# Performance work log

Measured on AMD Instinct MI355X. Metric: run time of the kernel, lower is better.

## Reference

```python
import jax, jax.numpy as jnp
import numpy as np

L = 3          # levels
B = 128        # batch
T0 = 256       # bottom-level sequence length
FACTOR = 4     # tmp_abs_factor -> T levels = [256, 64, 16]
STOCH = 128
DETER = 1024
EMBED = 512
OBS_D = 512    # obs_embed_size / enc_dense_embed_size


def setup_inputs() -> dict:
    key = jax.random.key(0)
    ks = jax.random.split(key, 16)
    w = lambda k, shape: jax.random.normal(k, shape, jnp.float32) * 0.02
    return {
        'obs_l0': jax.random.normal(ks[0], (B, T0, OBS_D), jnp.float32),
        'obs_l1': jax.random.normal(ks[1], (B, T0 // FACTOR, OBS_D), jnp.float32),
        'obs_l2': jax.random.normal(ks[2], (B, T0 // FACTOR**2, OBS_D), jnp.float32),
        # prior input dense: concat(prev_sample, context) -> embed
        'Wp': w(ks[3], (L, STOCH + DETER, EMBED)),
        'bp': jnp.zeros((L, EMBED), jnp.float32),
        # GRUCell (torch semantics): input=embed, hidden=deter
        'Wih': w(ks[4], (L, EMBED, 3 * DETER)),
        'Whh': w(ks[5], (L, DETER, 3 * DETER)),
        'bih': jnp.zeros((L, 3 * DETER), jnp.float32),
        'bhh': jnp.zeros((L, 3 * DETER), jnp.float32),
        # posterior dense: concat(det_out, obs) -> embed, then mean head -> stoch
        'Wq': w(ks[6], (L, DETER + OBS_D, EMBED)),
        'bq': jnp.zeros((L, EMBED), jnp.float32),
        'Wqm': w(ks[7], (L, EMBED, STOCH)),
        'bqm': jnp.zeros((L, STOCH), jnp.float32),
    }


def _gru(x, h, Wih, Whh, bih, bhh):
    # torch.nn.GRUCell math
    gi = x @ Wih + bih
    gh = h @ Whh + bhh
    ir, iz, inn = jnp.split(gi, 3, axis=-1)
    hr, hz, hn = jnp.split(gh, 3, axis=-1)
    r = jax.nn.sigmoid(ir + hr)
    z = jax.nn.sigmoid(iz + hz)
    n = jnp.tanh(inn + r * hn)
    return (1.0 - z) * n + z * h


def _run_level(obs, ctx, p):
    # one RSSMCell scanned over time; returns posterior det_out [B, T, DETER]
    Wp, bp, Wih, Whh, bih, bhh, Wq, bq, Wqm, bqm = p
    bsz = obs.shape[0]

    def step(carry, xt):
        sample, det = carry                       # [B,STOCH], [B,DETER]
        obs_t, ctx_t = xt                         # [B,OBS_D], [B,DETER]
        # prior: dense -> GRU (mean_only, so prior heads don't affect the state path)
        h = jax.nn.relu(jnp.concatenate([sample, ctx_t], -1) @ Wp + bp)
        det_new = _gru(h, det, Wih, Whh, bih, bhh)
        # posterior (use_observation=True): mean head gives next sample (mean_only cell)
        qh = jax.nn.relu(jnp.concatenate([det_new, obs_t], -1) @ Wq + bq)
        qm = qh @ Wqm + bqm
        return (qm, det_new), det_new

    init = (jnp.zeros((bsz, STOCH), obs.dtype), jnp.zeros((bsz, DETER), obs.dtype))
    xs = (jnp.swapaxes(obs, 0, 1), jnp.swapaxes(ctx, 0, 1))  # time-major
    _, dets = jax.lax.scan(step, init, xs)
    return jnp.swapaxes(dets, 0, 1)


def reference(obs_l0, obs_l1, obs_l2, Wp, bp, Wih, Whh, bih, bhh, Wq, bq, Wqm, bqm):
    obs = [obs_l0, obs_l1, obs_l2]
    bsz = obs_l0.shape[0]
    # top-level context is zeros of det-state size
    ctx = jnp.zeros((bsz, obs[L - 1].shape[1], DETER), obs_l0.dtype)
    for level in range(L - 1, -1, -1):
        o = obs[level]
        T = o.shape[1]
        if ctx.shape[1] < T:
            reps = -(-T // ctx.shape[1])  # ceil, matches torch repeat-then-slice
            ctx = jnp.tile(ctx, (1, reps, 1))[:, :T]
        ctx = ctx[:, :T]
        p = (Wp[level], bp[level], Wih[level], Whh[level], bih[level], bhh[level],
             Wq[level], bq[level], Wqm[level], bqm[level])
        ctx = _run_level(o, ctx, p)  # posterior det_out becomes next context
    return ctx  # output_bot_level [B, T0, DETER]
```

## Files before the change

kernel.cpp:

```cpp
#include <hip/hip_runtime.h>
#include <math.h>
#include <cstddef>

#define G3 3072

__device__ __forceinline__ float sigmoidf_(float x){ return 1.0f/(1.0f+expf(-x)); }

__global__ __launch_bounds__(256)
void zero_k(float* p, int n){
    int i = blockIdx.x*blockDim.x + threadIdx.x;
    for (int j = i; j < n; j += gridDim.x*blockDim.x) p[j] = 0.f;
}

__global__ __launch_bounds__(256)
void gemm_k(const float* __restrict__ A, long lda,
            const float* __restrict__ Bm, long ldb,
            const float* __restrict__ bias,
            float* __restrict__ C, long ldc, int K)
{
    __shared__ float xs[16][64];
    const int tid = threadIdx.x;
    const int nl = tid & 31, bl = tid >> 5;
    const int n  = blockIdx.x*64 + nl*2;
    const int m0 = blockIdx.y*16;
    float a0x=0.f,a0y=0.f,a1x=0.f,a1y=0.f;
    for (int kc = 0; kc < K; kc += 64) {
        __syncthreads();
        { int r = tid >> 4, c = (tid & 15)*4;
          *(float4*)&xs[r][c] = *(const float4*)&A[(size_t)(m0+r)*lda + kc + c]; }
        __syncthreads();
        #pragma unroll 8
        for (int kk = 0; kk < 64; ++kk) {
            const float2 w = *(const float2*)&Bm[(size_t)(kc+kk)*ldb + n];
            const float xa = xs[bl][kk], xb = xs[bl+8][kk];
            a0x += xa*w.x; a0y += xa*w.y;
            a1x += xb*w.x; a1y += xb*w.y;
        }
    }
    float bx=0.f, by=0.f;
    if (bias){ bx = bias[n]; by = bias[n+1]; }
    float* c0 = &C[(size_t)(m0+bl)*ldc + n];
    float* c1 = &C[(size_t)(m0+bl+8)*ldc + n];
    c0[0]=a0x+bx; c0[1]=a0y+by; c1[0]=a1x+bx; c1[1]=a1y+by;
}

__global__ __launch_bounds__(512)
void bps_k(const float* __restrict__ bqm, const float* __restrict__ Wps,
           const float* __restrict__ bp, float* __restrict__ bps)
{
    const int n = threadIdx.x;
    float a = 0.f;
    #pragma unroll 8
    for (int k = 0; k < 128; ++k) a += bqm[k]*Wps[(size_t)k*512 + n];
    bps[n] = a + bp[n];
}

__global__ __launch_bounds__(256)
void qh_part_k(const float* __restrict__ det, long ld_det,
               const float* __restrict__ obs, long ld_obs,
               const float* __restrict__ Wq,
               float* __restrict__ qp)
{
    __shared__ float xs[8][256];
    const int tid = threadIdx.x;
    const int nl = tid & 31, mg = tid >> 5;
    const int n  = blockIdx.x*64 + nl*2;
    const int m0 = blockIdx.y*8;
    const int cz = blockIdx.z;
    const float* As; long lda; int kr0;
    if (cz < 4) { As = det + cz*256;     lda = ld_det; kr0 = cz*256; }
    else        { As = obs + (cz-4)*256; lda = ld_obs; kr0 = 1024 + (cz-4)*256; }
    {
        const int r = tid >> 5, c = (tid & 31)*8;
        const float* src = &As[(size_t)(m0+r)*lda + c];
        *(float4*)&xs[r][c]   = *(const float4*)&src[0];
        *(float4*)&xs[r][c+4] = *(const float4*)&src[4];
    }
    __syncthreads();
    const float* w = &Wq[(size_t)kr0*512 + n];
    float ax=0.f, ay=0.f;
    #pragma unroll 8
    for (int kk = 0; kk < 256; ++kk) {
        const float2 wv = *(const float2*)&w[(size_t)kk*512];
        const float x = xs[mg][kk];
        ax += x*wv.x; ay += x*wv.y;
    }
    *(float2*)&qp[(size_t)cz*65536 + (size_t)(m0+mg)*512 + n] = make_float2(ax, ay);
}

__global__ __launch_bounds__(256)
void h_part_k(const float* __restrict__ qp, const float* __restrict__ bq,
              const float* __restrict__ Wqs, float* __restrict__ hp)
{
    __shared__ float xs[8][128];
    const int tid = threadIdx.x;
    const int nl = tid & 31, mg = tid >> 5;
    const int n  = blockIdx.x*64 + nl*2;
    const int m0 = blockIdx.y*8;
    const int kz = blockIdx.z;
    {
        const int r = tid >> 5, c = (tid & 31)*4;
        const int kg = kz*128 + c;
        float4 s = *(const float4*)&bq[kg];
        #pragma unroll
        for (int cc = 0; cc < 6; ++cc) {
            const float4 p = *(const float4*)&qp[(size_t)cc*65536 + (size_t)(m0+r)*512 + kg];
            s.x += p.x; s.y += p.y; s.z += p.z; s.w += p.w;
        }
        s.x = fmaxf(s.x,0.f); s.y = fmaxf(s.y,0.f);
        s.z = fmaxf(s.z,0.f); s.w = fmaxf(s.w,0.f);
        *(float4*)&xs[r][c] = s;
    }
    __syncthreads();
    const float* w = &Wqs[(size_t)(kz*128)*512 + n];
    float ax=0.f, ay=0.f;
    #pragma unroll 8
    for (int kk = 0; kk < 128; ++kk) {
        const float2 wv = *(const float2*)&w[(size_t)kk*512];
        const float x = xs[mg][kk];
        ax += x*wv.x; ay += x*wv.y;
    }
    *(float2*)&hp[(size_t)kz*65536 + (size_t)(m0+mg)*512 + n] = make_float2(ax, ay);
}

__global__ __launch_bounds__(256)
void gru_part_k(const float* __restrict__ hp,
                const float* __restrict__ hc, long ld_hc,
                const float* __restrict__ hbias,
                const float* __restrict__ det, long ld_det,
                const float* __restrict__ Wih, const float* __restrict__ Whh,
                float* __restrict__ giP, float* __restrict__ ghP)
{
    __shared__ float xs[32*132];
    const int tid = threadIdx.x;
    const int nl = tid & 31, mg = tid >> 5;
    const int n  = blockIdx.x*128 + nl*4;
    const int m0 = blockIdx.y*32;
    const int zc = blockIdx.z;
    const bool is_gi = (zc < 4);
    {
        const int r = tid >> 3, c0 = (tid & 7)*16;
        if (is_gi) {
            const int kb = zc*128;
            #pragma unroll
            for (int i = 0; i < 4; ++i) {
                const int c = c0 + i*4, kg = kb + c;
                float4 s = *(const float4*)&hbias[kg];
                if (hc) {
                    const float4 p = *(const float4*)&hc[(size_t)(m0+r)*ld_hc + kg];
                    s.x+=p.x; s.y+=p.y; s.z+=p.z; s.w+=p.w;
                }
                if (hp) {
                    #pragma unroll
                    for (int cc = 0; cc < 4; ++cc) {
                        const float4 p = *(const float4*)&hp[(size_t)cc*65536 + (size_t)(m0+r)*512 + kg];
                        s.x+=p.x; s.y+=p.y; s.z+=p.z; s.w+=p.w;
                    }
                }
                s.x=fmaxf(s.x,0.f); s.y=fmaxf(s.y,0.f);
                s.z=fmaxf(s.z,0.f); s.w=fmaxf(s.w,0.f);
                *(float4*)&xs[r*132 + c] = s;
            }
        } else {
            const int kb = (zc-4)*128;
            #pragma unroll
            for (int i = 0; i < 4; ++i) {
                const int c = c0 + i*4;
                *(float4*)&xs[r*132 + c] =
                    *(const float4*)&det[(size_t)(m0+r)*ld_det + kb + c];
            }
        }
    }
    __syncthreads();
    const float* W; float* outp;
    if (is_gi) { W = Wih + (size_t)(zc*128)*G3 + n;     outp = giP + (size_t)zc*393216; }
    else       { W = Whh + (size_t)((zc-4)*128)*G3 + n; outp = ghP + (size_t)(zc-4)*393216; }
    float4 acc[4];
    #pragma unroll
    for (int j = 0; j < 4; ++j) acc[j] = make_float4(0.f,0.f,0.f,0.f);
    const int rb = mg*4;
    #pragma unroll 2
    for (int kc4 = 0; kc4 < 128; kc4 += 4) {
        float4 xv[4];
        #pragma unroll
        for (int j = 0; j < 4; ++j)
            xv[j] = *(const float4*)&xs[(rb+j)*132 + kc4];
        #pragma unroll
        for (int kk = 0; kk < 4; ++kk) {
            const float4 wv = *(const float4*)&W[(size_t)(kc4+kk)*G3];
            #pragma unroll
            for (int j = 0; j < 4; ++j) {
                const float xj = (kk==0) ? xv[j].x : (kk==1) ? xv[j].y
                               : (kk==2) ? xv[j].z : xv[j].w;
                acc[j].x += xj*wv.x; acc[j].y += xj*wv.y;
                acc[j].z += xj*wv.z; acc[j].w += xj*wv.w;
            }
        }
    }
    #pragma unroll
    for (int j = 0; j < 4; ++j)
        *(float4*)&outp[(size_t)(m0+rb+j)*G3 + n] = acc[j];
}

__global__ __launch_bounds__(256)
void gru_epi_k(const float* __restrict__ giP, const float* __restrict__ ghP,
               const float* __restrict__ bih, const float* __restrict__ bhh,
               const float* __restrict__ det_in, long ld_det,
               float* __restrict__ det_out, long ld_out)
{
    const int d = blockIdx.x*256 + threadIdx.x;
    const int b = blockIdx.y;
    float gir=0.f, giz=0.f, gin=0.f;
    #pragma unroll
    for (int c = 0; c < 4; ++c) {
        const float* p = &giP[(size_t)c*393216 + (size_t)b*G3 + d];
        gir += p[0]; giz += p[1024]; gin += p[2048];
    }
    float ghr=0.f, ghz=0.f, ghn=0.f;
    #pragma unroll
    for (int c = 0; c < 8; ++c) {
        const float* p = &ghP[(size_t)c*393216 + (size_t)b*G3 + d];
        ghr += p[0]; ghz += p[1024]; ghn += p[2048];
    }
    const float r  = sigmoidf_(gir + ghr + bih[d] + bhh[d]);
    const float z  = sigmoidf_(giz + ghz + bih[1024+d] + bhh[1024+d]);
    const float nn = tanhf(gin + bih[2048+d] + r*(ghn + bhh[2048+d]));
    const float dold = det_in[(size_t)b*ld_det + d];
    det_out[(size_t)b*ld_out + d] = (1.f - z)*nn + z*dold;
}

extern "C" void kernel_launch(void* const* d_in, const int* in_sizes, int n_in,
                              void* d_out, int out_size, void* d_ws, size_t ws_size,
                              hipStream_t stream)
{
    const float* obs0 = (const float*)d_in[0];
    const float* obs1 = (const float*)d_in[1];
    const float* obs2 = (const float*)d_in[2];
    const float* Wp   = (const float*)d_in[3];
    const float* bp   = (const float*)d_in[4];
    const float* Wih  = (const float*)d_in[5];
    const float* Whh  = (const float*)d_in[6];
    const float* bih  = (const float*)d_in[7];
    const float* bhh  = (const float*)d_in[8];
    const float* Wq   = (const float*)d_in[9];
    const float* bq   = (const float*)d_in[10];
    const float* Wqm  = (const float*)d_in[11];
    const float* bqm  = (const float*)d_in[12];

    float* ws = (float*)d_ws;
    float* det0 = ws;  ws += (size_t)128*1024;
    float* WqsA = ws;  ws += (size_t)3*512*512;
    float* bpsA = ws;  ws += (size_t)3*512;
    float* dets2= ws;  ws += (size_t)128*16*1024;
    float* dets1= ws;  ws += (size_t)128*64*1024;
    float* HCu  = ws;  ws += (size_t)128*64*512;
    float* qp   = ws;  ws += (size_t)6*128*512;
    float* hp   = ws;  ws += (size_t)4*128*512;
    float* giP  = ws;  ws += (size_t)4*128*3072;
    float* ghP  = ws;  ws += (size_t)8*128*3072;

    zero_k<<<dim3(128), dim3(256), 0, stream>>>(det0, 128*1024);

    for (int l = 0; l < 3; ++l) {
        const float* Wp_l = Wp + (size_t)l*1152*512;
        gemm_k<<<dim3(8,32), dim3(256), 0, stream>>>(
            Wqm + (size_t)l*512*128, 128, Wp_l, 512, nullptr,
            WqsA + (size_t)l*512*512, 512, 128);
        bps_k<<<dim3(1), dim3(512), 0, stream>>>(
            bqm + (size_t)l*128, Wp_l, bp + (size_t)l*512, bpsA + (size_t)l*512);
    }

    const float* obsv[3] = {obs0, obs1, obs2};
    const int Tv[3] = {256, 64, 16};

    for (int level = 2; level >= 0; --level) {
        const int T = Tv[level];
        const float* o = obsv[level];
        float* dseq = (level == 0) ? (float*)d_out : (level == 1 ? dets1 : dets2);
        const float* ctxd = (level == 2) ? nullptr : (level == 1 ? dets2 : dets1);
        const int Tc = (level == 1) ? 16 : 64;

        const float* Wp_l  = Wp  + (size_t)level*1152*512;
        const float* Wpc_l = Wp_l + (size_t)128*512;
        const float* bp_l  = bp  + (size_t)level*512;
        const float* Wih_l = Wih + (size_t)level*512*3072;
        const float* Whh_l = Whh + (size_t)level*1024*3072;
        const float* bih_l = bih + (size_t)level*3072;
        const float* bhh_l = bhh + (size_t)level*3072;
        const float* Wq_l  = Wq  + (size_t)level*1536*512;
        const float* bq_l  = bq  + (size_t)level*512;
        const float* Wqs_l = WqsA + (size_t)level*512*512;
        const float* bps_l = bpsA + (size_t)level*512;

        if (level < 2) {
            gemm_k<<<dim3(8, (128*Tc)/16), dim3(256), 0, stream>>>(
                ctxd, 1024, Wpc_l, 512, nullptr, HCu, 512, 1024);
        }

        for (int t = 0; t < T; ++t) {
            if (t > 0) {
                qh_part_k<<<dim3(8,16,6), dim3(256), 0, stream>>>(
                    dseq + (size_t)(t-1)*1024, (long)T*1024,
                    o + (size_t)(t-1)*512,  (long)T*512, Wq_l, qp);
                h_part_k<<<dim3(8,16,4), dim3(256), 0, stream>>>(qp, bq_l, Wqs_l, hp);
            }
            const float* hc_t  = (level < 2) ? HCu + (size_t)(t % Tc)*512 : nullptr;
            const float* dprev = t ? dseq + (size_t)(t-1)*1024 : det0;
            const long   ldprev = t ? (long)T*1024 : 1024L;
            gru_part_k<<<dim3(24,4,12), dim3(256), 0, stream>>>(
                t ? hp : nullptr, hc_t, (long)Tc*512,
                t ? bps_l : bp_l, dprev, ldprev,
                Wih_l, Whh_l, giP, ghP);
            gru_epi_k<<<dim3(4,128), dim3(256), 0, stream>>>(
                giP, ghP, bih_l, bhh_l, dprev, ldprev,
                dseq + (size_t)t*1024, (long)T*1024);
        }
    }
}
```

Measured before the change: 23.47 ms.

## Move Whh GEMM into stepA and fuse GRU epilogue via last-block atomic counter

The recurrent h@Whh partial GEMM now runs in the same launch as the posterior qh GEMM, since both depend only on the previous det state. That shortens the dependent chain before the Wih GEMM. The GRU epilogue is folded into the Wih GEMM kernel: the last block to finish each output tile, detected with an atomic counter, reduces the partials and applies the gates. This removes one launch per step and the det0 zero buffer. The qh and h kernels are widened to float4 per thread. The cost is a single block doing a serial epilogue per tile, plus atomic and fence overhead.

```diff
diff --git a/kernel.cpp b/kernel.cpp
--- a/kernel.cpp
+++ b/kernel.cpp
@@ -5,6 +5,17 @@
 #define G3 3072
 
 __device__ __forceinline__ float sigmoidf_(float x){ return 1.0f/(1.0f+expf(-x)); }
+
+__device__ __forceinline__ float gru_out_(float gi_r,float gh_r,float bir,float bhr,
+                                          float gi_z,float gh_z,float biz,float bhz,
+                                          float gi_n,float gh_n,float bin,float bhn,
+                                          float dold)
+{
+    const float r = sigmoidf_(gi_r + gh_r + bir + bhr);
+    const float z = sigmoidf_(gi_z + gh_z + biz + bhz);
+    const float n = tanhf(gi_n + bin + r*(gh_n + bhn));
+    return (1.f - z)*n + z*dold;
+}
 
 __global__ __launch_bounds__(256)
 void zero_k(float* p, int n){
@@ -56,46 +67,96 @@
 }
 
 __global__ __launch_bounds__(256)
-void qh_part_k(const float* __restrict__ det, long ld_det,
-               const float* __restrict__ obs, long ld_obs,
-               const float* __restrict__ Wq,
-               float* __restrict__ qp)
-{
-    __shared__ float xs[8][256];
+void stepA_k(const float* __restrict__ det, long ld_det,
+             const float* __restrict__ obs, long ld_obs,
+             const float* __restrict__ Wq,
+             float* __restrict__ qp,
+             const float* __restrict__ Whh,
+             float* __restrict__ ghP)
+{
+    __shared__ float xs[32*132];
     const int tid = threadIdx.x;
-    const int nl = tid & 31, mg = tid >> 5;
-    const int n  = blockIdx.x*64 + nl*2;
-    const int m0 = blockIdx.y*8;
-    const int cz = blockIdx.z;
-    const float* As; long lda; int kr0;
-    if (cz < 4) { As = det + cz*256;     lda = ld_det; kr0 = cz*256; }
-    else        { As = obs + (cz-4)*256; lda = ld_obs; kr0 = 1024 + (cz-4)*256; }
-    {
-        const int r = tid >> 5, c = (tid & 31)*8;
-        const float* src = &As[(size_t)(m0+r)*lda + c];
-        *(float4*)&xs[r][c]   = *(const float4*)&src[0];
-        *(float4*)&xs[r][c+4] = *(const float4*)&src[4];
-    }
-    __syncthreads();
-    const float* w = &Wq[(size_t)kr0*512 + n];
-    float ax=0.f, ay=0.f;
-    #pragma unroll 8
-    for (int kk = 0; kk < 256; ++kk) {
-        const float2 wv = *(const float2*)&w[(size_t)kk*512];
-        const float x = xs[mg][kk];
-        ax += x*wv.x; ay += x*wv.y;
-    }
-    *(float2*)&qp[(size_t)cz*65536 + (size_t)(m0+mg)*512 + n] = make_float2(ax, ay);
+    const int bid = blockIdx.x;
+    if (bid < 384) {
+        const int x = bid & 3, y = (bid>>2)&15, cz = bid>>6;
+        const int nl = tid & 31, mg = tid >> 5;
+        const int n  = x*128 + nl*4;
+        const int m0 = y*8;
+        const float* As; long lda; int kr0;
+        if (cz < 4) { As = det + cz*256;     lda = ld_det; kr0 = cz*256; }
+        else        { As = obs + (cz-4)*256; lda = ld_obs; kr0 = 1024 + (cz-4)*256; }
+        {
+            const int r = tid >> 5, c = (tid & 31)*8;
+            const float* src = &As[(size_t)(m0+r)*lda + c];
+            *(float4*)&xs[r*256 + c]     = *(const float4*)&src[0];
+            *(float4*)&xs[r*256 + c + 4] = *(const float4*)&src[4];
+        }
+        __syncthreads();
+        const float* w = &Wq[(size_t)kr0*512 + n];
+        float4 acc = make_float4(0.f,0.f,0.f,0.f);
+        #pragma unroll 8
+        for (int kk = 0; kk < 256; ++kk) {
+            const float4 wv = *(const float4*)&w[(size_t)kk*512];
+            const float xv = xs[mg*256 + kk];
+            acc.x += xv*wv.x; acc.y += xv*wv.y;
+            acc.z += xv*wv.z; acc.w += xv*wv.w;
+        }
+        *(float4*)&qp[(size_t)cz*65536 + (size_t)(m0+mg)*512 + n] = acc;
+    } else {
+        const int g = bid - 384;
+        const int x = g % 24, y = (g/24)&3, zc = g/96;
+        const int nl = tid & 31, mg = tid >> 5;
+        const int n  = x*128 + nl*4;
+        const int m0 = y*32;
+        const int kb = zc*128;
+        {
+            const int r = tid >> 3, c0 = (tid & 7)*16;
+            #pragma unroll
+            for (int i = 0; i < 4; ++i) {
+                const int c = c0 + i*4;
+                *(float4*)&xs[r*132 + c] =
+                    *(const float4*)&det[(size_t)(m0+r)*ld_det + kb + c];
+            }
+        }
+        __syncthreads();
+        const float* W = Whh + (size_t)kb*G3 + n;
+        float* outp = ghP + (size_t)zc*393216;
+        float4 acc[4];
+        #pragma unroll
+        for (int j = 0; j < 4; ++j) acc[j] = make_float4(0.f,0.f,0.f,0.f);
+        const int rb = mg*4;
+        #pragma unroll 2
+        for (int kc4 = 0; kc4 < 128; kc4 += 4) {
+            float4 xv[4];
+            #pragma unroll
+            for (int j = 0; j < 4; ++j)
+                xv[j] = *(const float4*)&xs[(rb+j)*132 + kc4];
+            #pragma unroll
+            for (int kk = 0; kk < 4; ++kk) {
+                const float4 wv = *(const float4*)&W[(size_t)(kc4+kk)*G3];
+                #pragma unroll
+                for (int j = 0; j < 4; ++j) {
+                    const float xj = (kk==0) ? xv[j].x : (kk==1) ? xv[j].y
+                                   : (kk==2) ? xv[j].z : xv[j].w;
+                    acc[j].x += xj*wv.x; acc[j].y += xj*wv.y;
+                    acc[j].z += xj*wv.z; acc[j].w += xj*wv.w;
+                }
+            }
+        }
+        #pragma unroll
+        for (int j = 0; j < 4; ++j)
+            *(float4*)&outp[(size_t)(m0+rb+j)*G3 + n] = acc[j];
+    }
 }
 
 __global__ __launch_bounds__(256)
 void h_part_k(const float* __restrict__ qp, const float* __restrict__ bq,
               const float* __restrict__ Wqs, float* __restrict__ hp)
 {
-    __shared__ float xs[8][128];
+    __shared__ float xs[8*128];
     const int tid = threadIdx.x;
     const int nl = tid & 31, mg = tid >> 5;
-    const int n  = blockIdx.x*64 + nl*2;
+    const int n  = blockIdx.x*128 + nl*4;
     const int m0 = blockIdx.y*8;
     const int kz = blockIdx.z;
     {
@@ -109,124 +170,159 @@
         }
         s.x = fmaxf(s.x,0.f); s.y = fmaxf(s.y,0.f);
         s.z = fmaxf(s.z,0.f); s.w = fmaxf(s.w,0.f);
-        *(float4*)&xs[r][c] = s;
+        *(float4*)&xs[r*128 + c] = s;
     }
     __syncthreads();
     const float* w = &Wqs[(size_t)(kz*128)*512 + n];
-    float ax=0.f, ay=0.f;
+    float4 acc = make_float4(0.f,0.f,0.f,0.f);
     #pragma unroll 8
     for (int kk = 0; kk < 128; ++kk) {
-        const float2 wv = *(const float2*)&w[(size_t)kk*512];
-        const float x = xs[mg][kk];
-        ax += x*wv.x; ay += x*wv.y;
-    }
-    *(float2*)&hp[(size_t)kz*65536 + (size_t)(m0+mg)*512 + n] = make_float2(ax, ay);
+        const float4 wv = *(const float4*)&w[(size_t)kk*512];
+        const float xv = xs[mg*128 + kk];
+        acc.x += xv*wv.x; acc.y += xv*wv.y;
+        acc.z += xv*wv.z; acc.w += xv*wv.w;
+    }
+    *(float4*)&hp[(size_t)kz*65536 + (size_t)(m0+mg)*512 + n] = acc;
 }
 
 __global__ __launch_bounds__(256)
-void gru_part_k(const float* __restrict__ hp,
-                const float* __restrict__ hc, long ld_hc,
-                const float* __restrict__ hbias,
-                const float* __restrict__ det, long ld_det,
-                const float* __restrict__ Wih, const float* __restrict__ Whh,
-                float* __restrict__ giP, float* __restrict__ ghP)
+void stepC_k(const float* __restrict__ hp,
+             const float* __restrict__ hc, long ld_hc,
+             const float* __restrict__ hbias,
+             const float* __restrict__ det_in, long ld_det,
+             const float* __restrict__ Wih,
+             float* __restrict__ giP,
+             const float* __restrict__ ghP,
+             const float* __restrict__ bih, const float* __restrict__ bhh,
+             float* __restrict__ det_out, long ld_out,
+             int have_gh, int* __restrict__ cnt)
 {
     __shared__ float xs[32*132];
+    __shared__ int last;
     const int tid = threadIdx.x;
+    const int x = blockIdx.x, y = blockIdx.y, zc = blockIdx.z;
     const int nl = tid & 31, mg = tid >> 5;
-    const int n  = blockIdx.x*128 + nl*4;
-    const int m0 = blockIdx.y*32;
-    const int zc = blockIdx.z;
-    const bool is_gi = (zc < 4);
+    const int n  = x*128 + nl*4;
+    const int m0 = y*32;
     {
         const int r = tid >> 3, c0 = (tid & 7)*16;
-        if (is_gi) {
-            const int kb = zc*128;
-            #pragma unroll
-            for (int i = 0; i < 4; ++i) {
-                const int c = c0 + i*4, kg = kb + c;
-                float4 s = *(const float4*)&hbias[kg];
-                if (hc) {
-                    const float4 p = *(const float4*)&hc[(size_t)(m0+r)*ld_hc + kg];
+        const int kb = zc*128;
+        #pragma unroll
+        for (int i = 0; i < 4; ++i) {
+            const int c = c0 + i*4, kg = kb + c;
+            float4 s = *(const float4*)&hbias[kg];
+            if (hc) {
+                const float4 p = *(const float4*)&hc[(size_t)(m0+r)*ld_hc + kg];
+                s.x+=p.x; s.y+=p.y; s.z+=p.z; s.w+=p.w;
+            }
+            if (hp) {
+                #pragma unroll
+                for (int cc = 0; cc < 4; ++cc) {
+                    const float4 p = *(const float4*)&hp[(size_t)cc*65536 + (size_t)(m0+r)*512 + kg];
                     s.x+=p.x; s.y+=p.y; s.z+=p.z; s.w+=p.w;
                 }
-                if (hp) {
-                    #pragma unroll
-                    for (int cc = 0; cc < 4; ++cc) {
-                        const float4 p = *(const float4*)&hp[(size_t)cc*65536 + (size_t)(m0+r)*512 + kg];
-                        s.x+=p.x; s.y+=p.y; s.z+=p.z; s.w+=p.w;
-                    }
+            }
+            s.x=fmaxf(s.x,0.f); s.y=fmaxf(s.y,0.f);
+            s.z=fmaxf(s.z,0.f); s.w=fmaxf(s.w,0.f);
+            *(float4*)&xs[r*132 + c] = s;
+        }
+    }
+    __syncthreads();
+    {
+        const float* W = Wih + (size_t)(zc*128)*G3 + n;
+        float* outp = giP + (size_t)zc*393216;
+        float4 acc[4];
+        #pragma unroll
+        for (int j = 0; j < 4; ++j) acc[j] = make_float4(0.f,0.f,0.f,0.f);
+        const int rb = mg*4;
+        #pragma unroll 2
+        for (int kc4 = 0; kc4 < 128; kc4 += 4) {
+            float4 xv[4];
+            #pragma unroll
+            for (int j = 0; j < 4; ++j)
+                xv[j] = *(const float4*)&xs[(rb+j)*132 + kc4];
+            #pragma unroll
+            for (int kk = 0; kk < 4; ++kk) {
+                const float4 wv = *(const float4*)&W[(size_t)(kc4+kk)*G3];
+                #pragma unroll
+                for (int j = 0; j < 4; ++j) {
+                    const float xj = (kk==0) ? xv[j].x : (kk==1) ? xv[j].y
+                                   : (kk==2) ? xv[j].z : xv[j].w;
+                    acc[j].x += xj*wv.x; acc[j].y += xj*wv.y;
+                    acc[j].z += xj*wv.z; acc[j].w += xj*wv.w;
                 }
-                s.x=fmaxf(s.x,0.f); s.y=fmaxf(s.y,0.f);
-                s.z=fmaxf(s.z,0.f); s.w=fmaxf(s.w,0.f);
-                *(float4*)&xs[r*132 + c] = s;
-            }
-        } else {
-            const int kb = (zc-4)*128;
-            #pragma unroll
-            for (int i = 0; i < 4; ++i) {
-                const int c = c0 + i*4;
-                *(float4*)&xs[r*132 + c] =
-                    *(const float4*)&det[(size_t)(m0+r)*ld_det + kb + c];
-            }
-        }
-    }
+            }
+        }
+        #pragma unroll
+        for (int j = 0; j < 4; ++j)
+            *(float4*)&outp[(size_t)(m0+rb+j)*G3 + n] = acc[j];
+    }
+
+    __threadfence();
     __syncthreads();
-    const float* W; float* outp;
-    if (is_gi) { W = Wih + (size_t)(zc*128)*G3 + n;     outp = giP + (size_t)zc*393216; }
-    else       { W = Whh + (size_t)((zc-4)*128)*G3 + n; outp = ghP + (size_t)(zc-4)*393216; }
-    float4 acc[4];
-    #pragma unroll
-    for (int j = 0; j < 4; ++j) acc[j] = make_float4(0.f,0.f,0.f,0.f);
-    const int rb = mg*4;
-    #pragma unroll 2
-    for (int kc4 = 0; kc4 < 128; kc4 += 4) {
-        float4 xv[4];
-        #pragma unroll
-        for (int j = 0; j < 4; ++j)
-            xv[j] = *(const float4*)&xs[(rb+j)*132 + kc4];
-        #pragma unroll
-        for (int kk = 0; kk < 4; ++kk) {
-            const float4 wv = *(const float4*)&W[(size_t)(kc4+kk)*G3];
-            #pragma unroll
-            for (int j = 0; j < 4; ++j) {
-                const float xj = (kk==0) ? xv[j].x : (kk==1) ? xv[j].y
-                               : (kk==2) ? xv[j].z : xv[j].w;
-                acc[j].x += xj*wv.x; acc[j].y += xj*wv.y;
-                acc[j].z += xj*wv.z; acc[j].w += xj*wv.w;
-            }
-        }
-    }
-    #pragma unroll
-    for (int j = 0; j < 4; ++j)
-        *(float4*)&outp[(size_t)(m0+rb+j)*G3 + n] = acc[j];
-}
-
-__global__ __launch_bounds__(256)
-void gru_epi_k(const float* __restrict__ giP, const float* __restrict__ ghP,
-               const float* __restrict__ bih, const float* __restrict__ bhh,
-               const float* __restrict__ det_in, long ld_det,
-               float* __restrict__ det_out, long ld_out)
-{
-    const int d = blockIdx.x*256 + threadIdx.x;
-    const int b = blockIdx.y;
-    float gir=0.f, giz=0.f, gin=0.f;
-    #pragma unroll
-    for (int c = 0; c < 4; ++c) {
-        const float* p = &giP[(size_t)c*393216 + (size_t)b*G3 + d];
-        gir += p[0]; giz += p[1024]; gin += p[2048];
-    }
-    float ghr=0.f, ghz=0.f, ghn=0.f;
-    #pragma unroll
-    for (int c = 0; c < 8; ++c) {
-        const float* p = &ghP[(size_t)c*393216 + (size_t)b*G3 + d];
-        ghr += p[0]; ghz += p[1024]; ghn += p[2048];
-    }
-    const float r  = sigmoidf_(gir + ghr + bih[d] + bhh[d]);
-    const float z  = sigmoidf_(giz + ghz + bih[1024+d] + bhh[1024+d]);
-    const float nn = tanhf(gin + bih[2048+d] + r*(ghn + bhh[2048+d]));
-    const float dold = det_in[(size_t)b*ld_det + d];
-    det_out[(size_t)b*ld_out + d] = (1.f - z)*nn + z*dold;
+    const int dx = x & 7;
+    const int ci = y*8 + dx;
+    if (tid == 0) {
+        int old = __hip_atomic_fetch_add(&cnt[ci], 1, __ATOMIC_ACQ_REL,
+                                         __HIP_MEMORY_SCOPE_AGENT);
+        last = (old == 11);
+    }
+    __syncthreads();
+    if (!last) return;
+    if (tid == 0)
+        __hip_atomic_store(&cnt[ci], 0, __ATOMIC_RELAXED, __HIP_MEMORY_SCOPE_AGENT);
+    __threadfence();
+
+    const int d0 = dx*128 + (tid & 31)*4;
+    const float4 bir = *(const float4*)&bih[d0];
+    const float4 bhr = *(const float4*)&bhh[d0];
+    const float4 biz = *(const float4*)&bih[1024+d0];
+    const float4 bhz = *(const float4*)&bhh[1024+d0];
+    const float4 bin = *(const float4*)&bih[2048+d0];
+    const float4 bhn = *(const float4*)&bhh[2048+d0];
+    for (int rr = tid >> 5; rr < 32; rr += 8) {
+        const int b = m0 + rr;
+        float4 gr = make_float4(0.f,0.f,0.f,0.f);
+        float4 gz = make_float4(0.f,0.f,0.f,0.f);
+        float4 gn = make_float4(0.f,0.f,0.f,0.f);
+        #pragma unroll
+        for (int c = 0; c < 4; ++c) {
+            const float* p = &giP[(size_t)c*393216 + (size_t)b*G3 + d0];
+            const float4 a = *(const float4*)&p[0];
+            gr.x+=a.x; gr.y+=a.y; gr.z+=a.z; gr.w+=a.w;
+            const float4 bb = *(const float4*)&p[1024];
+            gz.x+=bb.x; gz.y+=bb.y; gz.z+=bb.z; gz.w+=bb.w;
+            const float4 cc = *(const float4*)&p[2048];
+            gn.x+=cc.x; gn.y+=cc.y; gn.z+=cc.z; gn.w+=cc.w;
+        }
+        float4 hr = make_float4(0.f,0.f,0.f,0.f);
+        float4 hz = make_float4(0.f,0.f,0.f,0.f);
+        float4 hn = make_float4(0.f,0.f,0.f,0.f);
+        float4 dold = make_float4(0.f,0.f,0.f,0.f);
+        if (have_gh) {
+            #pragma unroll
+            for (int c = 0; c < 8; ++c) {
+                const float* p = &ghP[(size_t)c*393216 + (size_t)b*G3 + d0];
+                const float4 a = *(const float4*)&p[0];
+                hr.x+=a.x; hr.y+=a.y; hr.z+=a.z; hr.w+=a.w;
+                const float4 bb = *(const float4*)&p[1024];
+                hz.x+=bb.x; hz.y+=bb.y; hz.z+=bb.z; hz.w+=bb.w;
+                const float4 cc = *(const float4*)&p[2048];
+                hn.x+=cc.x; hn.y+=cc.y; hn.z+=cc.z; hn.w+=cc.w;
+            }
+            dold = *(const float4*)&det_in[(size_t)b*ld_det + d0];
+        }
+        float4 out;
+        out.x = gru_out_(gr.x,hr.x,bir.x,bhr.x, gz.x,hz.x,biz.x,bhz.x,
+                         gn.x,hn.x,bin.x,bhn.x, dold.x);
+        out.y = gru_out_(gr.y,hr.y,bir.y,bhr.y, gz.y,hz.y,biz.y,bhz.y,
+                         gn.y,hn.y,bin.y,bhn.y, dold.y);
+        out.z = gru_out_(gr.z,hr.z,bir.z,bhr.z, gz.z,hz.z,biz.z,bhz.z,
+                         gn.z,hn.z,bin.z,bhn.z, dold.z);
+        out.w = gru_out_(gr.w,hr.w,bir.w,bhr.w, gz.w,hz.w,biz.w,bhz.w,
+                         gn.w,hn.w,bin.w,bhn.w, dold.w);
+        *(float4*)&det_out[(size_t)b*ld_out + d0] = out;
+    }
 }
 
 extern "C" void kernel_launch(void* const* d_in, const int* in_sizes, int n_in,
@@ -248,7 +344,7 @@
     const float* bqm  = (const float*)d_in[12];
 
     float* ws = (float*)d_ws;
-    float* det0 = ws;  ws += (size_t)128*1024;
+    int*   cnt  = (int*)ws;  ws += 1024;
     float* WqsA = ws;  ws += (size_t)3*512*512;
     float* bpsA = ws;  ws += (size_t)3*512;
     float* dets2= ws;  ws += (size_t)128*16*1024;
@@ -259,7 +355,7 @@
     float* giP  = ws;  ws += (size_t)4*128*3072;
     float* ghP  = ws;  ws += (size_t)8*128*3072;
 
-    zero_k<<<dim3(128), dim3(256), 0, stream>>>(det0, 128*1024);
+    zero_k<<<dim3(1), dim3(256), 0, stream>>>((float*)cnt, 1024);
 
     for (int l = 0; l < 3; ++l) {
         const float* Wp_l = Wp + (size_t)l*1152*512;
@@ -298,22 +394,20 @@
         }
 
         for (int t = 0; t < T; ++t) {
+            const float* dprev = t ? dseq + (size_t)(t-1)*1024 : dseq;
+            const long   ldd   = (long)T*1024;
             if (t > 0) {
-                qh_part_k<<<dim3(8,16,6), dim3(256), 0, stream>>>(
-                    dseq + (size_t)(t-1)*1024, (long)T*1024,
-                    o + (size_t)(t-1)*512,  (long)T*512, Wq_l, qp);
-                h_part_k<<<dim3(8,16,4), dim3(256), 0, stream>>>(qp, bq_l, Wqs_l, hp);
-            }
-            const float* hc_t  = (level < 2) ? HCu + (size_t)(t % Tc)*512 : nullptr;
-            const float* dprev = t ? dseq + (size_t)(t-1)*1024 : det0;
-            const long   ldprev = t ? (long)T*1024 : 1024L;
-            gru_part_k<<<dim3(24,4,12), dim3(256), 0, stream>>>(
+                stepA_k<<<dim3(1152), dim3(256), 0, stream>>>(
+                    dprev, ldd, o + (size_t)(t-1)*512, (long)T*512,
+                    Wq_l, qp, Whh_l, ghP);
+                h_part_k<<<dim3(4,16,4), dim3(256), 0, stream>>>(qp, bq_l, Wqs_l, hp);
+            }
+            const float* hc_t = (level < 2) ? HCu + (size_t)(t % Tc)*512 : nullptr;
+            stepC_k<<<dim3(24,4,4), dim3(256), 0, stream>>>(
                 t ? hp : nullptr, hc_t, (long)Tc*512,
-                t ? bps_l : bp_l, dprev, ldprev,
-                Wih_l, Whh_l, giP, ghP);
-            gru_epi_k<<<dim3(4,128), dim3(256), 0, stream>>>(
-                giP, ghP, bih_l, bhh_l, dprev, ldprev,
-                dseq + (size_t)t*1024, (long)T*1024);
-        }
-    }
-}
+                t ? bps_l : bp_l, dprev, ldd,
+                Wih_l, giP, ghP, bih_l, bhh_l,
+                dseq + (size_t)t*1024, ldd, t > 0 ? 1 : 0, cnt);
+        }
+    }
+}
```

New measurement: 40.36 ms. 1.72x slower.

## Reschedule GRU step: run Whh matmul alongside Wq, fuse Wih matmul into epilogue

Applied to the files above, without the earlier changes.

The hidden-state matmul (det @ Whh) only depends on the previous state, so it moves into the same launch as the posterior Wq partial products. The input-gate matmul (h @ Wih) is fused with the GRU nonlinearity epilogue in one kernel, which removes the giP partial buffer and the separate epilogue launch. The zero-init kernel is dropped by special-casing t=0, and the posterior kernels widen to float4 outputs. Per timestep this goes from four launches to three and less intermediate traffic, but the fused Wih kernel runs only 256 blocks each doing the full K=512 reduction, which may give lower parallelism.

```diff
diff --git a/kernel.cpp b/kernel.cpp
--- a/kernel.cpp
+++ b/kernel.cpp
@@ -5,12 +5,6 @@
 #define G3 3072
 
 __device__ __forceinline__ float sigmoidf_(float x){ return 1.0f/(1.0f+expf(-x)); }
-
-__global__ __launch_bounds__(256)
-void zero_k(float* p, int n){
-    int i = blockIdx.x*blockDim.x + threadIdx.x;
-    for (int j = i; j < n; j += gridDim.x*blockDim.x) p[j] = 0.f;
-}
 
 __global__ __launch_bounds__(256)
 void gemm_k(const float* __restrict__ A, long lda,
@@ -56,46 +50,96 @@
 }
 
 __global__ __launch_bounds__(256)
-void qh_part_k(const float* __restrict__ det, long ld_det,
-               const float* __restrict__ obs, long ld_obs,
-               const float* __restrict__ Wq,
-               float* __restrict__ qp)
-{
-    __shared__ float xs[8][256];
+void stepA_k(const float* __restrict__ det, long ld_det,
+             const float* __restrict__ obs, long ld_obs,
+             const float* __restrict__ Wq,
+             float* __restrict__ qp,
+             const float* __restrict__ Whh,
+             float* __restrict__ ghP)
+{
+    __shared__ float xs[32*132];
     const int tid = threadIdx.x;
-    const int nl = tid & 31, mg = tid >> 5;
-    const int n  = blockIdx.x*64 + nl*2;
-    const int m0 = blockIdx.y*8;
-    const int cz = blockIdx.z;
-    const float* As; long lda; int kr0;
-    if (cz < 4) { As = det + cz*256;     lda = ld_det; kr0 = cz*256; }
-    else        { As = obs + (cz-4)*256; lda = ld_obs; kr0 = 1024 + (cz-4)*256; }
-    {
-        const int r = tid >> 5, c = (tid & 31)*8;
-        const float* src = &As[(size_t)(m0+r)*lda + c];
-        *(float4*)&xs[r][c]   = *(const float4*)&src[0];
-        *(float4*)&xs[r][c+4] = *(const float4*)&src[4];
-    }
-    __syncthreads();
-    const float* w = &Wq[(size_t)kr0*512 + n];
-    float ax=0.f, ay=0.f;
-    #pragma unroll 8
-    for (int kk = 0; kk < 256; ++kk) {
-        const float2 wv = *(const float2*)&w[(size_t)kk*512];
-        const float x = xs[mg][kk];
-        ax += x*wv.x; ay += x*wv.y;
-    }
-    *(float2*)&qp[(size_t)cz*65536 + (size_t)(m0+mg)*512 + n] = make_float2(ax, ay);
+    const int bid = blockIdx.x;
+    if (bid < 384) {
+        const int x = bid & 3, y = (bid>>2)&15, cz = bid>>6;
+        const int nl = tid & 31, mg = tid >> 5;
+        const int n  = x*128 + nl*4;
+        const int m0 = y*8;
+        const float* As; long lda; int kr0;
+        if (cz < 4) { As = det + cz*256;     lda = ld_det; kr0 = cz*256; }
+        else        { As = obs + (cz-4)*256; lda = ld_obs; kr0 = 1024 + (cz-4)*256; }
+        {
+            const int r = tid >> 5, c = (tid & 31)*8;
+            const float* src = &As[(size_t)(m0+r)*lda + c];
+            *(float4*)&xs[r*256 + c]     = *(const float4*)&src[0];
+            *(float4*)&xs[r*256 + c + 4] = *(const float4*)&src[4];
+        }
+        __syncthreads();
+        const float* w = &Wq[(size_t)kr0*512 + n];
+        float4 acc = make_float4(0.f,0.f,0.f,0.f);
+        #pragma unroll 8
+        for (int kk = 0; kk < 256; ++kk) {
+            const float4 wv = *(const float4*)&w[(size_t)kk*512];
+            const float xv = xs[mg*256 + kk];
+            acc.x += xv*wv.x; acc.y += xv*wv.y;
+            acc.z += xv*wv.z; acc.w += xv*wv.w;
+        }
+        *(float4*)&qp[(size_t)cz*65536 + (size_t)(m0+mg)*512 + n] = acc;
+    } else {
+        const int g = bid - 384;
+        const int x = g % 24, y = (g/24)&3, zc = g/96;
+        const int nl = tid & 31, mg = tid >> 5;
+        const int n  = x*128 + nl*4;
+        const int m0 = y*32;
+        const int kb = zc*128;
+        {
+            const int r = tid >> 3, c0 = (tid & 7)*16;
+            #pragma unroll
+            for (int i = 0; i < 4; ++i) {
+                const int c = c0 + i*4;
+                *(float4*)&xs[r*132 + c] =
+                    *(const float4*)&det[(size_t)(m0+r)*ld_det + kb + c];
+            }
+        }
+        __syncthreads();
+        const float* W = Whh + (size_t)kb*G3 + n;
+        float* outp = ghP + (size_t)zc*393216;
+        float4 acc[4];
+        #pragma unroll
+        for (int j = 0; j < 4; ++j) acc[j] = make_float4(0.f,0.f,0.f,0.f);
+        const int rb = mg*4;
+        #pragma unroll 2
+        for (int kc4 = 0; kc4 < 128; kc4 += 4) {
+            float4 xv[4];
+            #pragma unroll
+            for (int j = 0; j < 4; ++j)
+                xv[j] = *(const float4*)&xs[(rb+j)*132 + kc4];
+            #pragma unroll
+            for (int kk = 0; kk < 4; ++kk) {
+                const float4 wv = *(const float4*)&W[(size_t)(kc4+kk)*G3];
+                #pragma unroll
+                for (int j = 0; j < 4; ++j) {
+                    const float xj = (kk==0) ? xv[j].x : (kk==1) ? xv[j].y
+                                   : (kk==2) ? xv[j].z : xv[j].w;
+                    acc[j].x += xj*wv.x; acc[j].y += xj*wv.y;
+                    acc[j].z += xj*wv.z; acc[j].w += xj*wv.w;
+                }
+            }
+        }
+        #pragma unroll
+        for (int j = 0; j < 4; ++j)
+            *(float4*)&outp[(size_t)(m0+rb+j)*G3 + n] = acc[j];
+    }
 }
 
 __global__ __launch_bounds__(256)
 void h_part_k(const float* __restrict__ qp, const float* __restrict__ bq,
               const float* __restrict__ Wqs, float* __restrict__ hp)
 {
-    __shared__ float xs[8][128];
+    __shared__ float xs[8*128];
     const int tid = threadIdx.x;
     const int nl = tid & 31, mg = tid >> 5;
-    const int n  = blockIdx.x*64 + nl*2;
+    const int n  = blockIdx.x*128 + nl*4;
     const int m0 = blockIdx.y*8;
     const int kz = blockIdx.z;
     {
@@ -109,124 +153,112 @@
         }
         s.x = fmaxf(s.x,0.f); s.y = fmaxf(s.y,0.f);
         s.z = fmaxf(s.z,0.f); s.w = fmaxf(s.w,0.f);
-        *(float4*)&xs[r][c] = s;
+        *(float4*)&xs[r*128 + c] = s;
     }
     __syncthreads();
     const float* w = &Wqs[(size_t)(kz*128)*512 + n];
-    float ax=0.f, ay=0.f;
+    float4 acc = make_float4(0.f,0.f,0.f,0.f);
     #pragma unroll 8
     for (int kk = 0; kk < 128; ++kk) {
-        const float2 wv = *(const float2*)&w[(size_t)kk*512];
-        const float x = xs[mg][kk];
-        ax += x*wv.x; ay += x*wv.y;
-    }
-    *(float2*)&hp[(size_t)kz*65536 + (size_t)(m0+mg)*512 + n] = make_float2(ax, ay);
+        const float4 wv = *(const float4*)&w[(size_t)kk*512];
+        const float xv = xs[mg*128 + kk];
+        acc.x += xv*wv.x; acc.y += xv*wv.y;
+        acc.z += xv*wv.z; acc.w += xv*wv.w;
+    }
+    *(float4*)&hp[(size_t)kz*65536 + (size_t)(m0+mg)*512 + n] = acc;
 }
 
 __global__ __launch_bounds__(256)
-void gru_part_k(const float* __restrict__ hp,
-                const float* __restrict__ hc, long ld_hc,
-                const float* __restrict__ hbias,
-                const float* __restrict__ det, long ld_det,
-                const float* __restrict__ Wih, const float* __restrict__ Whh,
-                float* __restrict__ giP, float* __restrict__ ghP)
-{
-    __shared__ float xs[32*132];
+void stepC_k(const float* __restrict__ hp,
+             const float* __restrict__ hc, long ld_hc,
+             const float* __restrict__ hbias,
+             const float* __restrict__ det_in, long ld_det,
+             const float* __restrict__ Wih,
+             const float* __restrict__ ghP,
+             const float* __restrict__ bih, const float* __restrict__ bhh,
+             float* __restrict__ det_out, long ld_out,
+             int have_gh)
+{
+    __shared__ float xs[8*512];
     const int tid = threadIdx.x;
     const int nl = tid & 31, mg = tid >> 5;
-    const int n  = blockIdx.x*128 + nl*4;
-    const int m0 = blockIdx.y*32;
-    const int zc = blockIdx.z;
-    const bool is_gi = (zc < 4);
+    const int d  = blockIdx.x*64 + nl*2;
+    const int b0 = blockIdx.y*8;
     {
-        const int r = tid >> 3, c0 = (tid & 7)*16;
-        if (is_gi) {
-            const int kb = zc*128;
-            #pragma unroll
-            for (int i = 0; i < 4; ++i) {
-                const int c = c0 + i*4, kg = kb + c;
-                float4 s = *(const float4*)&hbias[kg];
-                if (hc) {
-                    const float4 p = *(const float4*)&hc[(size_t)(m0+r)*ld_hc + kg];
+        const int r = tid >> 5, cl = (tid & 31)*4;
+        #pragma unroll
+        for (int pass = 0; pass < 4; ++pass) {
+            const int kg = pass*128 + cl;
+            float4 s = *(const float4*)&hbias[kg];
+            if (hc) {
+                const float4 p = *(const float4*)&hc[(size_t)(b0+r)*ld_hc + kg];
+                s.x+=p.x; s.y+=p.y; s.z+=p.z; s.w+=p.w;
+            }
+            if (hp) {
+                #pragma unroll
+                for (int cc = 0; cc < 4; ++cc) {
+                    const float4 p = *(const float4*)&hp[(size_t)cc*65536 + (size_t)(b0+r)*512 + kg];
                     s.x+=p.x; s.y+=p.y; s.z+=p.z; s.w+=p.w;
                 }
-                if (hp) {
-                    #pragma unroll
-                    for (int cc = 0; cc < 4; ++cc) {
-                        const float4 p = *(const float4*)&hp[(size_t)cc*65536 + (size_t)(m0+r)*512 + kg];
-                        s.x+=p.x; s.y+=p.y; s.z+=p.z; s.w+=p.w;
-                    }
-                }
-                s.x=fmaxf(s.x,0.f); s.y=fmaxf(s.y,0.f);
-                s.z=fmaxf(s.z,0.f); s.w=fmaxf(s.w,0.f);
-                *(float4*)&xs[r*132 + c] = s;
-            }
-        } else {
-            const int kb = (zc-4)*128;
-            #pragma unroll
-            for (int i = 0; i < 4; ++i) {
-                const int c = c0 + i*4;
-                *(float4*)&xs[r*132 + c] =
-                    *(const float4*)&det[(size_t)(m0+r)*ld_det + kb + c];
-            }
+            }
+            s.x=fmaxf(s.x,0.f); s.y=fmaxf(s.y,0.f);
+            s.z=fmaxf(s.z,0.f); s.w=fmaxf(s.w,0.f);
+            *(float4*)&xs[r*512 + kg] = s;
         }
     }
     __syncthreads();
-    const float* W; float* outp;
-    if (is_gi) { W = Wih + (size_t)(zc*128)*G3 + n;     outp = giP + (size_t)zc*393216; }
-    else       { W = Whh + (size_t)((zc-4)*128)*G3 + n; outp = ghP + (size_t)(zc-4)*393216; }
-    float4 acc[4];
-    #pragma unroll
-    for (int j = 0; j < 4; ++j) acc[j] = make_float4(0.f,0.f,0.f,0.f);
-    const int rb = mg*4;
-    #pragma unroll 2
-    for (int kc4 = 0; kc4 < 128; kc4 += 4) {
-        float4 xv[4];
-        #pragma unroll
-        for (int j = 0; j < 4; ++j)
-            xv[j] = *(const float4*)&xs[(rb+j)*132 + kc4];
-        #pragma unroll
-        for (int kk = 0; kk < 4; ++kk) {
-            const float4 wv = *(const float4*)&W[(size_t)(kc4+kk)*G3];
-            #pragma unroll
-            for (int j = 0; j < 4; ++j) {
-                const float xj = (kk==0) ? xv[j].x : (kk==1) ? xv[j].y
-                               : (kk==2) ? xv[j].z : xv[j].w;
-                acc[j].x += xj*wv.x; acc[j].y += xj*wv.y;
-                acc[j].z += xj*wv.z; acc[j].w += xj*wv.w;
-            }
-        }
-    }
-    #pragma unroll
-    for (int j = 0; j < 4; ++j)
-        *(float4*)&outp[(size_t)(m0+rb+j)*G3 + n] = acc[j];
-}
-
-__global__ __launch_bounds__(256)
-void gru_epi_k(const float* __restrict__ giP, const float* __restrict__ ghP,
-               const float* __restrict__ bih, const float* __restrict__ bhh,
-               const float* __restrict__ det_in, long ld_det,
-               float* __restrict__ det_out, long ld_out)
-{
-    const int d = blockIdx.x*256 + threadIdx.x;
-    const int b = blockIdx.y;
-    float gir=0.f, giz=0.f, gin=0.f;
-    #pragma unroll
-    for (int c = 0; c < 4; ++c) {
-        const float* p = &giP[(size_t)c*393216 + (size_t)b*G3 + d];
-        gir += p[0]; giz += p[1024]; gin += p[2048];
-    }
-    float ghr=0.f, ghz=0.f, ghn=0.f;
-    #pragma unroll
-    for (int c = 0; c < 8; ++c) {
-        const float* p = &ghP[(size_t)c*393216 + (size_t)b*G3 + d];
-        ghr += p[0]; ghz += p[1024]; ghn += p[2048];
-    }
-    const float r  = sigmoidf_(gir + ghr + bih[d] + bhh[d]);
-    const float z  = sigmoidf_(giz + ghz + bih[1024+d] + bhh[1024+d]);
-    const float nn = tanhf(gin + bih[2048+d] + r*(ghn + bhh[2048+d]));
-    const float dold = det_in[(size_t)b*ld_det + d];
-    det_out[(size_t)b*ld_out + d] = (1.f - z)*nn + z*dold;
+
+    float2 ar = make_float2(0.f,0.f);
+    float2 az = make_float2(0.f,0.f);
+    float2 an = make_float2(0.f,0.f);
+    const float* Wb = Wih + d;
+    #pragma unroll 4
+    for (int k = 0; k < 512; ++k) {
+        const float xv = xs[mg*512 + k];
+        const float* w = Wb + (size_t)k*G3;
+        const float2 wr = *(const float2*)w;
+        const float2 wz = *(const float2*)(w + 1024);
+        const float2 wn = *(const float2*)(w + 2048);
+        ar.x += xv*wr.x; ar.y += xv*wr.y;
+        az.x += xv*wz.x; az.y += xv*wz.y;
+        an.x += xv*wn.x; an.y += xv*wn.y;
+    }
+
+    const int b = b0 + mg;
+    float2 hr = make_float2(0.f,0.f);
+    float2 hz = make_float2(0.f,0.f);
+    float2 hn = make_float2(0.f,0.f);
+    float2 dold = make_float2(0.f,0.f);
+    if (have_gh) {
+        #pragma unroll
+        for (int c = 0; c < 8; ++c) {
+            const float* p = &ghP[(size_t)c*393216 + (size_t)b*G3 + d];
+            const float2 a2 = *(const float2*)p;
+            hr.x += a2.x; hr.y += a2.y;
+            const float2 b2 = *(const float2*)(p + 1024);
+            hz.x += b2.x; hz.y += b2.y;
+            const float2 c2 = *(const float2*)(p + 2048);
+            hn.x += c2.x; hn.y += c2.y;
+        }
+        dold = *(const float2*)&det_in[(size_t)b*ld_det + d];
+    }
+    const float2 brI = *(const float2*)&bih[d];
+    const float2 brH = *(const float2*)&bhh[d];
+    const float2 bzI = *(const float2*)&bih[1024+d];
+    const float2 bzH = *(const float2*)&bhh[1024+d];
+    const float2 bnI = *(const float2*)&bih[2048+d];
+    const float2 bnH = *(const float2*)&bhh[2048+d];
+
+    const float rx = sigmoidf_(ar.x + hr.x + brI.x + brH.x);
+    const float ry = sigmoidf_(ar.y + hr.y + brI.y + brH.y);
+    const float zx = sigmoidf_(az.x + hz.x + bzI.x + bzH.x);
+    const float zy = sigmoidf_(az.y + hz.y + bzI.y + bzH.y);
+    const float nx = tanhf(an.x + bnI.x + rx*(hn.x + bnH.x));
+    const float ny = tanhf(an.y + bnI.y + ry*(hn.y + bnH.y));
+    float2 dn;
+    dn.x = (1.f - zx)*nx + zx*dold.x;
+    dn.y = (1.f - zy)*ny + zy*dold.y;
+    *(float2*)&det_out[(size_t)b*ld_out + d] = dn;
 }
 
 extern "C" void kernel_launch(void* const* d_in, const int* in_sizes, int n_in,
@@ -248,7 +280,6 @@
     const float* bqm  = (const float*)d_in[12];
 
     float* ws = (float*)d_ws;
-    float* det0 = ws;  ws += (size_t)128*1024;
     float* WqsA = ws;  ws += (size_t)3*512*512;
     float* bpsA = ws;  ws += (size_t)3*512;
     float* dets2= ws;  ws += (size_t)128*16*1024;
@@ -256,10 +287,7 @@
     float* HCu  = ws;  ws += (size_t)128*64*512;
     float* qp   = ws;  ws += (size_t)6*128*512;
     float* hp   = ws;  ws += (size_t)4*128*512;
-    float* giP  = ws;  ws += (size_t)4*128*3072;
     float* ghP  = ws;  ws += (size_t)8*128*3072;
-
-    zero_k<<<dim3(128), dim3(256), 0, stream>>>(det0, 128*1024);
 
     for (int l = 0; l < 3; ++l) {
         const float* Wp_l = Wp + (size_t)l*1152*512;
@@ -298,22 +326,20 @@
         }
 
         for (int t = 0; t < T; ++t) {
+            const float* dprev = t ? dseq + (size_t)(t-1)*1024 : dseq;
+            const long   ldd   = (long)T*1024;
             if (t > 0) {
-                qh_part_k<<<dim3(8,16,6), dim3(256), 0, stream>>>(
-                    dseq + (size_t)(t-1)*1024, (long)T*1024,
-                    o + (size_t)(t-1)*512,  (long)T*512, Wq_l, qp);
-                h_part_k<<<dim3(8,16,4), dim3(256), 0, stream>>>(qp, bq_l, Wqs_l, hp);
-            }
-            const float* hc_t  = (level < 2) ? HCu + (size_t)(t % Tc)*512 : nullptr;
-            const float* dprev = t ? dseq + (size_t)(t-1)*1024 : det0;
-            const long   ldprev = t ? (long)T*1024 : 1024L;
-            gru_part_k<<<dim3(24,4,12), dim3(256), 0, stream>>>(
+                stepA_k<<<dim3(1152), dim3(256), 0, stream>>>(
+                    dprev, ldd, o + (size_t)(t-1)*512, (long)T*512,
+                    Wq_l, qp, Whh_l, ghP);
+                h_part_k<<<dim3(4,16,4), dim3(256), 0, stream>>>(qp, bq_l, Wqs_l, hp);
+            }
+            const float* hc_t = (level < 2) ? HCu + (size_t)(t % Tc)*512 : nullptr;
+            stepC_k<<<dim3(16,16), dim3(256), 0, stream>>>(
                 t ? hp : nullptr, hc_t, (long)Tc*512,
-                t ? bps_l : bp_l, dprev, ldprev,
-                Wih_l, Whh_l, giP, ghP);
-            gru_epi_k<<<dim3(4,128), dim3(256), 0, stream>>>(
-                giP, ghP, bih_l, bhh_l, dprev, ldprev,
-                dseq + (size_t)t*1024, (long)T*1024);
-        }
-    }
-}
+                t ? bps_l : bp_l, dprev, ldd,
+                Wih_l, ghP, bih_l, bhh_l,
+                dseq + (size_t)t*1024, ldd, t > 0 ? 1 : 0);
+        }
+    }
+}
```

Result: slower. 34.53 ms (+47.1%).
